# Performance work log

Hardware: AMD Instinct MI355X
Metric: run time of the kernel (lower is better)

## Reference

```python
import jax, jax.numpy as jnp
import numpy as np

# Mamba hyperparams implied by Mamba(d_model=256, d_state=16, d_conv=4), expand=2 default
D_MODEL = 256
D_INNER = 512      # expand * d_model
D_STATE = 16
D_CONV = 4
DT_RANK = 16       # ceil(d_model / 16)
LN_EPS = 1e-5


def setup_inputs() -> dict:
    key = jax.random.key(0)
    ks = jax.random.split(key, 10)
    B, L = 4, 2048
    s = lambda k, shape, sc=0.02: jax.random.normal(k, shape, dtype=jnp.float32) * sc
    x = jax.random.normal(ks[0], (B, L, D_MODEL), dtype=jnp.float32)
    in_proj_w = s(ks[1], (2 * D_INNER, D_MODEL))          # Linear(d_model -> 2*d_inner), no bias
    conv_w = s(ks[2], (D_INNER, 1, D_CONV), 0.1)          # depthwise causal conv
    conv_b = s(ks[3], (D_INNER,), 0.1)
    x_proj_w = s(ks[4], (DT_RANK + 2 * D_STATE, D_INNER))  # Linear(d_inner -> dt_rank+2*d_state), no bias
    dt_proj_w = s(ks[5], (D_INNER, DT_RANK), 0.1)
    dt_proj_b = s(ks[6], (D_INNER,), 0.1)
    # S4D-real init: A_log = log(1..d_state) broadcast over channels
    A_log = jnp.log(jnp.tile(jnp.arange(1, D_STATE + 1, dtype=jnp.float32), (D_INNER, 1)))
    D_param = jnp.ones((D_INNER,), dtype=jnp.float32)
    out_proj_w = s(ks[7], (D_MODEL, D_INNER))             # Linear(d_inner -> d_model), no bias
    ln_w = jnp.ones((D_MODEL,), dtype=jnp.float32)
    ln_b = jnp.zeros((D_MODEL,), dtype=jnp.float32)
    return dict(x=x, in_proj_w=in_proj_w, conv_w=conv_w, conv_b=conv_b,
                x_proj_w=x_proj_w, dt_proj_w=dt_proj_w, dt_proj_b=dt_proj_b,
                A_log=A_log, D_param=D_param, out_proj_w=out_proj_w,
                ln_w=ln_w, ln_b=ln_b)


def _mamba(x, in_proj_w, conv_w, conv_b, x_proj_w, dt_proj_w, dt_proj_b, A_log, D_param, out_proj_w):
    B, L, _ = x.shape
    # input projection -> (x_branch, z_gate), each [B, L, E]
    xz = jnp.einsum('bld,ed->ble', x, in_proj_w)
    xm, z = jnp.split(xz, 2, axis=-1)
    # causal depthwise conv over time: [B, E, L]
    xc = jnp.transpose(xm, (0, 2, 1))
    xc = jax.lax.conv_general_dilated(xc, conv_w, window_strides=(1,),
                                      padding=[(D_CONV - 1, 0)],
                                      feature_group_count=D_INNER)
    xc = jax.nn.silu(xc + conv_b[None, :, None])
    xt = jnp.transpose(xc, (0, 2, 1))                     # [B, L, E]
    # SSM parameter projections
    dbc = jnp.einsum('ble,re->blr', xt, x_proj_w)         # [B, L, R+2N]
    dt, Bm, Cm = jnp.split(dbc, [DT_RANK, DT_RANK + D_STATE], axis=-1)
    delta = jax.nn.softplus(jnp.einsum('blr,er->ble', dt, dt_proj_w) + dt_proj_b)  # [B,L,E]
    A = -jnp.exp(A_log)                                   # [E, N]
    dA = jnp.exp(jnp.einsum('ble,en->blen', delta, A))    # [B,L,E,N]
    dBu = jnp.einsum('ble,bln->blen', delta * xt, Bm)     # [B,L,E,N]

    def step(h, inp):
        dA_t, dBu_t, C_t = inp                            # [B,E,N],[B,E,N],[B,N]
        h = dA_t * h + dBu_t
        y = jnp.einsum('ben,bn->be', h, C_t)
        return h, y

    h0 = jnp.zeros((B, D_INNER, D_STATE), dtype=x.dtype)
    xs = (jnp.moveaxis(dA, 1, 0), jnp.moveaxis(dBu, 1, 0), jnp.moveaxis(Cm, 1, 0))
    _, ys = jax.lax.scan(step, h0, xs)                    # ys: [L, B, E]
    y = jnp.moveaxis(ys, 0, 1) + xt * D_param             # skip term D*u
    y = y * jax.nn.silu(z)                                # gating
    return jnp.einsum('ble,de->bld', y, out_proj_w)


def reference(x, in_proj_w, conv_w, conv_b, x_proj_w, dt_proj_w, dt_proj_b,
              A_log, D_param, out_proj_w, ln_w, ln_b):
    xr = x + _mamba(x, in_proj_w, conv_w, conv_b, x_proj_w, dt_proj_w,
                    dt_proj_b, A_log, D_param, out_proj_w)
    mu = jnp.mean(xr, axis=-1, keepdims=True)
    var = jnp.mean(jnp.square(xr - mu), axis=-1, keepdims=True)
    ln = (xr - mu) * jax.lax.rsqrt(var + LN_EPS) * ln_w + ln_b
    return jnp.transpose(ln, (0, 2, 1))                   # [B, d_model, L]
```

## Files before the change

kernel.cpp:

```cpp
#include <hip/hip_runtime.h>

typedef __attribute__((ext_vector_type(8))) short short8;
typedef __attribute__((ext_vector_type(4))) float f32x4;

#define DMODEL 256
#define DINNER 512
#define NSTATE 16
#define LSEQ   2048
#define NB     4
#define BL     (NB*LSEQ)
#define NCHUNK 128
#define LCHUNK 16

#define NX     (BL*DMODEL)
#define NWIN   (1024*256)
#define NWXP   (64*512)
#define NWOUT  (256*512)

__device__ __forceinline__ ushort f2bf(float f) {
  union { float f; unsigned u; } v; v.f = f;
  unsigned u = v.u;
  unsigned r = (u + 0x7fffu + ((u >> 16) & 1u)) >> 16;
  return (ushort)r;
}
__device__ __forceinline__ float bf2f(ushort u) {
  union { unsigned u; float f; } v; v.u = ((unsigned)u) << 16; return v.f;
}

__device__ __forceinline__ void gld_lds16(const ushort* g, ushort* l) {
  __builtin_amdgcn_global_load_lds(
      (const __attribute__((address_space(1))) void*)g,
      (__attribute__((address_space(3))) void*)l, 16, 0, 0);
}

__global__ __launch_bounds__(256) void cvt_all_k(const float* __restrict__ x,
                                                 const float* __restrict__ w_in,
                                                 const float* __restrict__ w_xp,
                                                 const float* __restrict__ w_out,
                                                 ushort* __restrict__ xbf,
                                                 ushort* __restrict__ winb,
                                                 ushort* __restrict__ wxpb,
                                                 ushort* __restrict__ woutb) {
  int i = blockIdx.x * 256 + threadIdx.x;
  if (i < NX) { xbf[i] = f2bf(x[i]); return; }
  i -= NX;
  if (i < NWIN) { winb[i] = f2bf(w_in[i]); return; }
  i -= NWIN;
  if (i < NWXP) { wxpb[i] = ((i >> 9) < 48) ? f2bf(w_xp[i]) : (ushort)0; return; }
  i -= NWXP;
  if (i < NWOUT) woutb[i] = f2bf(w_out[i]);
}

__device__ __forceinline__ float sp(float s) {
  float ex = __expf(-fabsf(s));
  return fmaxf(s, 0.f) + __logf(1.f + ex);
}

__global__ __launch_bounds__(256) void inproj_conv_k(
    const ushort* __restrict__ A,
    const ushort* __restrict__ W,
    const float* __restrict__ x,
    const float* __restrict__ cw,
    const float* __restrict__ cb,
    ushort* __restrict__ xtbf,
    ushort* __restrict__ zsil) {
  constexpr int BM = 128, BN = 64, K = 256, NT = 4;
  constexpr int AL = BM / 8;
  constexpr int TL = (BM + BN) / 8;
  __shared__ __align__(16) char smem[48 * 1024 + 3 * 64 * 4];
  ushort* lA = (ushort*)smem;
  ushort* lB = (ushort*)(smem + 32768);
  float*  hal = (float*)(smem + 49152);
  const int t    = threadIdx.x;
  const int lane = t & 63;
  const int wave = t >> 6;
  const int wr = (wave >> 1) * 64;
  const int wc = (wave & 1) * 32;
  const int m0 = blockIdx.x * BM;
  const int n0 = blockIdx.y * BN;
  const bool xm_mode = (n0 < DINNER);
  const int lrow = lane >> 3;
  const int lcol = (lane & 7) * 8;

  f32x4 acc[4][2];
#pragma unroll
  for (int i = 0; i < 4; ++i)
#pragma unroll
    for (int j = 0; j < 2; ++j) acc[i][j] = (f32x4){0.f, 0.f, 0.f, 0.f};

  auto stage = [&](int buf, int kt64) {
#pragma unroll
    for (int li = 0; li < TL / 4; ++li) {
      int i = li * 4 + wave;
      if (i < AL) {
        int r = i * 8 + lrow;
        gld_lds16(A + (size_t)(m0 + r) * K + kt64 + lcol, &lA[buf * 8192 + i * 512]);
      } else {
        int r = (i - AL) * 8 + lrow;
        gld_lds16(W + (size_t)(n0 + r) * K + kt64 + lcol, &lB[buf * 4096 + (i - AL) * 512]);
      }
    }
  };

  stage(0, 0);
  if (xm_mode && t < 192) {
    int h = t >> 6, col = t & 63;
    float a = 0.f;
    if ((m0 & (LSEQ - 1)) != 0) {
      const float*  xr = x + (size_t)(m0 - 3 + h) * K;
      const ushort* wrp = W + (size_t)(n0 + col) * K;
      for (int k = 0; k < K; k += 4) {
        float4  xv = *reinterpret_cast<const float4*>(xr + k);
        ushort4 wv = *reinterpret_cast<const ushort4*>(wrp + k);
        a += xv.x * bf2f(wv.x) + xv.y * bf2f(wv.y)
           + xv.z * bf2f(wv.z) + xv.w * bf2f(wv.w);
      }
    }
    hal[h * 64 + col] = a;
  }
  __syncthreads();
  for (int kt = 0; kt < NT; ++kt) {
    const int cur = kt & 1;
    if (kt + 1 < NT) stage(cur ^ 1, (kt + 1) * 64);
#pragma unroll
    for (int kk = 0; kk < 64; kk += 32) {
      const int ko = kk + (lane >> 4) * 8;
      const int rr = lane & 15;
      short8 af[4], bf[2];
#pragma unroll
      for (int i = 0; i < 4; ++i)
        af[i] = *reinterpret_cast<const short8*>(&lA[cur * 8192 + (wr + i * 16 + rr) * 64 + ko]);
#pragma unroll
      for (int j = 0; j < 2; ++j)
        bf[j] = *reinterpret_cast<const short8*>(&lB[cur * 4096 + (wc + j * 16 + rr) * 64 + ko]);
#pragma unroll
      for (int i = 0; i < 4; ++i)
#pragma unroll
        for (int j = 0; j < 2; ++j)
          acc[i][j] = __builtin_amdgcn_mfma_f32_16x16x32_bf16(af[i], bf[j], acc[i][j], 0, 0, 0);
    }
    __syncthreads();
  }
  const int crow = (lane >> 4) * 4;
  const int ccol = lane & 15;

  if (xm_mode) {
    float* tile = (float*)smem;
#pragma unroll
    for (int i = 0; i < 4; ++i)
#pragma unroll
      for (int j = 0; j < 2; ++j)
#pragma unroll
        for (int r = 0; r < 4; ++r)
          tile[(wr + i * 16 + crow + r) * 66 + wc + j * 16 + ccol] = acc[i][j][r];
    __syncthreads();
    const int col = t & 63;
    const int e = n0 + col;
    float4 wq = reinterpret_cast<const float4*>(cw)[e];
    float bias = cb[e];
#pragma unroll 4
    for (int s = 0; s < 32; ++s) {
      int tok = (t >> 6) + s * 4;
      float v0 = tile[tok * 66 + col];
      float v1 = (tok >= 1) ? tile[(tok - 1) * 66 + col] : hal[(tok + 2) * 64 + col];
      float v2 = (tok >= 2) ? tile[(tok - 2) * 66 + col] : hal[(tok + 1) * 64 + col];
      float v3 = (tok >= 3) ? tile[(tok - 3) * 66 + col] : hal[(tok + 0) * 64 + col];
      float sv = bias + v0 * wq.w + v1 * wq.z + v2 * wq.y + v3 * wq.x;
      float sil = sv / (1.f + __expf(-sv));
      xtbf[(size_t)(m0 + tok) * DINNER + e] = f2bf(sil);
    }
  } else {
    const int zc0 = n0 - DINNER;
#pragma unroll
    for (int i = 0; i < 4; ++i)
#pragma unroll
      for (int j = 0; j < 2; ++j) {
        int row = m0 + wr + i * 16 + crow;
        int col = zc0 + wc + j * 16 + ccol;
#pragma unroll
        for (int r = 0; r < 4; ++r) {
          float v = acc[i][j][r];
          zsil[(size_t)(row + r) * DINNER + col] = f2bf(v / (1.f + __expf(-v)));
        }
      }
  }
}

template<int BM, int BN, int WM, int WN, int BF16OUT>
__global__ __launch_bounds__(256) void gemm_db(const ushort* __restrict__ A,
                                               const ushort* __restrict__ W,
                                               void* __restrict__ Cv,
                                               int M, int N, int K) {
  constexpr int FM = BM / WM / 16;
  constexpr int FN = BN / WN / 16;
  constexpr int AL = BM / 8;
  constexpr int TL = (BM + BN) / 8;
  __shared__ __align__(16) ushort lA[2][BM * 64];
  __shared__ __align__(16) ushort lB[2][BN * 64];
  const int t    = threadIdx.x;
  const int lane = t & 63;
  const int wave = t >> 6;
  const int wm = wave / WN, wn = wave % WN;
  const int wr = wm * (BM / WM);
  const int wc = wn * (BN / WN);
  const int m0 = blockIdx.x * BM;
  const int n0 = blockIdx.y * BN;
  const int lrow = lane >> 3;
  const int lcol = (lane & 7) * 8;

  f32x4 acc[FM][FN];
#pragma unroll
  for (int i = 0; i < FM; ++i)
#pragma unroll
    for (int j = 0; j < FN; ++j) acc[i][j] = (f32x4){0.f, 0.f, 0.f, 0.f};

  auto stage = [&](int buf, int kt64) {
#pragma unroll
    for (int li = 0; li < TL / 4; ++li) {
      int i = li * 4 + wave;
      if (i < AL) {
        int r = i * 8 + lrow;
        gld_lds16(A + (size_t)(m0 + r) * K + kt64 + lcol, &lA[buf][i * 512]);
      } else {
        int r = (i - AL) * 8 + lrow;
        gld_lds16(W + (size_t)(n0 + r) * K + kt64 + lcol, &lB[buf][(i - AL) * 512]);
      }
    }
  };

  const int NT = K / 64;
  stage(0, 0);
  __syncthreads();
  for (int kt = 0; kt < NT; ++kt) {
    const int cur = kt & 1;
    if (kt + 1 < NT) stage(cur ^ 1, (kt + 1) * 64);
#pragma unroll
    for (int kk = 0; kk < 64; kk += 32) {
      const int ko = kk + (lane >> 4) * 8;
      const int rr = lane & 15;
      short8 af[FM], bf[FN];
#pragma unroll
      for (int i = 0; i < FM; ++i)
        af[i] = *reinterpret_cast<const short8*>(&lA[cur][(wr + i * 16 + rr) * 64 + ko]);
#pragma unroll
      for (int j = 0; j < FN; ++j)
        bf[j] = *reinterpret_cast<const short8*>(&lB[cur][(wc + j * 16 + rr) * 64 + ko]);
#pragma unroll
      for (int i = 0; i < FM; ++i)
#pragma unroll
        for (int j = 0; j < FN; ++j)
          acc[i][j] = __builtin_amdgcn_mfma_f32_16x16x32_bf16(af[i], bf[j], acc[i][j], 0, 0, 0);
    }
    __syncthreads();
  }
  const int crow = (lane >> 4) * 4;
  const int ccol = lane & 15;
#pragma unroll
  for (int i = 0; i < FM; ++i)
#pragma unroll
    for (int j = 0; j < FN; ++j) {
      int row = m0 + wr + i * 16 + crow;
      int col = n0 + wc + j * 16 + ccol;
      if (BF16OUT) {
        ushort* C = (ushort*)Cv;
#pragma unroll
        for (int r = 0; r < 4; ++r)
          C[(size_t)(row + r) * N + col] = f2bf(acc[i][j][r]);
      } else {
        float* C = (float*)Cv;
#pragma unroll
        for (int r = 0; r < 4; ++r)
          C[(size_t)(row + r) * N + col] = acc[i][j][r];
      }
    }
}

__global__ __launch_bounds__(256) void outproj_ln_tr_k(
    const ushort* __restrict__ A,
    const ushort* __restrict__ W,
    const float* __restrict__ x,
    const float* __restrict__ lw,
    const float* __restrict__ lb,
    float* __restrict__ out) {
  constexpr int BM = 32, BN = 256, K = 512;
  constexpr int FM = 2, FN = 4;
  constexpr int AL = BM / 8;
  constexpr int TL = (BM + BN) / 8;
  __shared__ __align__(16) ushort lA[2][BM * 64];
  __shared__ __align__(16) ushort lB[2][BN * 64];
  const int t    = threadIdx.x;
  const int lane = t & 63;
  const int wave = t >> 6;
  const int wc = wave * 64;
  const int m0 = blockIdx.x * BM;
  const int lrow = lane >> 3;
  const int lcol = (lane & 7) * 8;

  f32x4 acc[FM][FN];
#pragma unroll
  for (int i = 0; i < FM; ++i)
#pragma unroll
    for (int j = 0; j < FN; ++j) acc[i][j] = (f32x4){0.f, 0.f, 0.f, 0.f};

  auto stage = [&](int buf, int kt64) {
#pragma unroll
    for (int li = 0; li < TL / 4; ++li) {
      int i = li * 4 + wave;
      if (i < AL) {
        int r = i * 8 + lrow;
        gld_lds16(A + (size_t)(m0 + r) * K + kt64 + lcol, &lA[buf][i * 512]);
      } else {
        int r = (i - AL) * 8 + lrow;
        gld_lds16(W + (size_t)r * K + kt64 + lcol, &lB[buf][(i - AL) * 512]);
      }
    }
  };

  const int NT = K / 64;
  stage(0, 0);
  __syncthreads();
  for (int kt = 0; kt < NT; ++kt) {
    const int cur = kt & 1;
    if (kt + 1 < NT) stage(cur ^ 1, (kt + 1) * 64);
#pragma unroll
    for (int kk = 0; kk < 64; kk += 32) {
      const int ko = kk + (lane >> 4) * 8;
      const int rr = lane & 15;
      short8 af[FM], bf[FN];
#pragma unroll
      for (int i = 0; i < FM; ++i)
        af[i] = *reinterpret_cast<const short8*>(&lA[cur][(i * 16 + rr) * 64 + ko]);
#pragma unroll
      for (int j = 0; j < FN; ++j)
        bf[j] = *reinterpret_cast<const short8*>(&lB[cur][(wc + j * 16 + rr) * 64 + ko]);
#pragma unroll
      for (int i = 0; i < FM; ++i)
#pragma unroll
        for (int j = 0; j < FN; ++j)
          acc[i][j] = __builtin_amdgcn_mfma_f32_16x16x32_bf16(af[i], bf[j], acc[i][j], 0, 0, 0);
    }
    __syncthreads();
  }

  float (*tile)[257] = reinterpret_cast<float (*)[257]>(&lB[0][0]);
  const int crow = (lane >> 4) * 4;
  const int ccol = lane & 15;
#pragma unroll
  for (int i = 0; i < FM; ++i)
#pragma unroll
    for (int j = 0; j < FN; ++j)
#pragma unroll
      for (int r = 0; r < 4; ++r)
        tile[i * 16 + crow + r][wc + j * 16 + ccol] = acc[i][j][r];
  __syncthreads();

  const int b = m0 / LSEQ, l0 = m0 % LSEQ;
  float4 w4 = *reinterpret_cast<const float4*>(lw + lane * 4);
  float4 b4 = *reinterpret_cast<const float4*>(lb + lane * 4);
#pragma unroll
  for (int s = 0; s < 8; ++s) {
    int row = wave * 8 + s;
    float4 xv = *reinterpret_cast<const float4*>(
        x + ((size_t)(b * LSEQ) + l0 + row) * DMODEL + lane * 4);
    float4 v;
    v.x = xv.x + tile[row][lane * 4 + 0];
    v.y = xv.y + tile[row][lane * 4 + 1];
    v.z = xv.z + tile[row][lane * 4 + 2];
    v.w = xv.w + tile[row][lane * 4 + 3];
    float sm = v.x + v.y + v.z + v.w;
    float ss = v.x * v.x + v.y * v.y + v.z * v.z + v.w * v.w;
#pragma unroll
    for (int o = 1; o < 64; o <<= 1) {
      sm += __shfl_xor(sm, o, 64);
      ss += __shfl_xor(ss, o, 64);
    }
    float mu = sm * (1.f / 256.f);
    float var = ss * (1.f / 256.f) - mu * mu;
    float rs = rsqrtf(var + 1e-5f);
    tile[row][lane * 4 + 0] = (v.x - mu) * rs * w4.x + b4.x;
    tile[row][lane * 4 + 1] = (v.y - mu) * rs * w4.y + b4.y;
    tile[row][lane * 4 + 2] = (v.z - mu) * rs * w4.z + b4.z;
    tile[row][lane * 4 + 3] = (v.w - mu) * rs * w4.w + b4.w;
  }
  __syncthreads();
  int l_i = t & 31;
  int dg = t >> 5;
  size_t ob = (size_t)b * DMODEL * LSEQ + l0 + l_i;
#pragma unroll
  for (int d = dg; d < DMODEL; d += 8)
    out[ob + (size_t)d * LSEQ] = tile[l_i][d];
}

__global__ __launch_bounds__(512) void dlt_k(const float* __restrict__ dbc,
                                             const float* __restrict__ dtw,
                                             const float* __restrict__ dtb,
                                             ushort* __restrict__ dlt) {
  int tg = blockIdx.x;
  int e = threadIdx.x;
  __shared__ float sDt[16][16];
  if (e < 256) {
    int li = e >> 4, n = e & 15;
    sDt[li][n] = dbc[((size_t)tg * 16 + li) * 64 + n];
  }
  const float4* wv = reinterpret_cast<const float4*>(dtw + e * 16);
  float4 w0 = wv[0], w1 = wv[1], w2 = wv[2], w3 = wv[3];
  float bias = dtb[e];
  __syncthreads();
  size_t ob = (size_t)tg * 16 * DINNER + e;
#pragma unroll
  for (int i = 0; i < 16; ++i) {
    float s = bias
      + w0.x*sDt[i][0]  + w0.y*sDt[i][1]  + w0.z*sDt[i][2]  + w0.w*sDt[i][3]
      + w1.x*sDt[i][4]  + w1.y*sDt[i][5]  + w1.z*sDt[i][6]  + w1.w*sDt[i][7]
      + w2.x*sDt[i][8]  + w2.y*sDt[i][9]  + w2.z*sDt[i][10] + w2.w*sDt[i][11]
      + w3.x*sDt[i][12] + w3.y*sDt[i][13] + w3.z*sDt[i][14] + w3.w*sDt[i][15];
    dlt[ob + (size_t)i * DINNER] = f2bf(sp(s));
  }
}

__global__ __launch_bounds__(256) void scanA_k(const ushort* __restrict__ xtbf,
                                               const ushort* __restrict__ dlt,
                                               const float* __restrict__ dbc,
                                               const float* __restrict__ A_log,
                                               ushort* __restrict__ hend,
                                               float* __restrict__ Ssum) {
  int blk = blockIdx.x;
  int half = blk & 1, c = (blk >> 1) & (NCHUNK - 1), b = blk >> 8;
  int e = half * 256 + threadIdx.x;
  __shared__ float sB[LCHUNK][NSTATE];
  {
    int t = threadIdx.x;
    int li = t >> 4, n = t & 15;
    sB[li][n] = dbc[((size_t)(b * LSEQ + c * LCHUNK + li)) * 64 + 16 + n];
  }
  float An0 = -__expf(A_log[e * 16]);
  float h[16];
#pragma unroll
  for (int n = 0; n < 16; ++n) h[n] = 0.f;
  float ssum = 0.f;
  __syncthreads();
  size_t ix = ((size_t)(b * LSEQ + c * LCHUNK)) * DINNER + e;
#pragma unroll
  for (int i = 0; i < LCHUNK; ++i, ix += DINNER) {
    float d = bf2f(dlt[ix]);
    float u = bf2f(xtbf[ix]);
    float du = d * u;
    ssum += d;
    float w = __expf(An0 * d);
    float w2 = w * w, w3 = w2 * w, w4 = w2 * w2;
    float c1 = w, c2 = w2, c3 = w3, c4 = w4;
#pragma unroll
    for (int q = 0; q < 4; ++q) {
      h[q*4+0] = c1 * h[q*4+0] + du * sB[i][q*4+0];
      h[q*4+1] = c2 * h[q*4+1] + du * sB[i][q*4+1];
      h[q*4+2] = c3 * h[q*4+2] + du * sB[i][q*4+2];
      h[q*4+3] = c4 * h[q*4+3] + du * sB[i][q*4+3];
      if (q < 3) { c1 *= w4; c2 *= w4; c3 *= w4; c4 *= w4; }
    }
  }
  size_t ob = ((size_t)b * NCHUNK + c) * DINNER + e;
  ushort tmp[16];
#pragma unroll
  for (int n = 0; n < 16; ++n) tmp[n] = f2bf(h[n]);
  *reinterpret_cast<uint4*>(hend + ob * 16)     = *reinterpret_cast<uint4*>(tmp);
  *reinterpret_cast<uint4*>(hend + ob * 16 + 8) = *reinterpret_cast<uint4*>(tmp + 8);
  Ssum[ob] = ssum;
}

__global__ __launch_bounds__(256) void scanB_k(ushort* hend,
                                               const float* __restrict__ Ssum,
                                               const float* __restrict__ A_log) {
  int idx = blockIdx.x * 256 + threadIdx.x;
  int n = idx & 15, e = (idx >> 4) & (DINNER - 1), b = idx >> 13;
  float An = -__expf(A_log[e * 16 + n]);
  float hc = 0.f;
#pragma unroll 8
  for (int c = 0; c < NCHUNK; ++c) {
    size_t base = ((size_t)b * NCHUNK + c) * DINNER + e;
    float s  = Ssum[base];
    float he = bf2f(hend[base * 16 + n]);
    hend[base * 16 + n] = f2bf(hc);
    hc = __expf(An * s) * hc + he;
  }
}

__global__ __launch_bounds__(256) void scanC_k(const ushort* __restrict__ xtbf,
                                               const ushort* __restrict__ dlt,
                                               const float* __restrict__ dbc,
                                               const float* __restrict__ A_log,
                                               const ushort* __restrict__ hin,
                                               const float* __restrict__ Dp,
                                               const ushort* __restrict__ zsil,
                                               ushort* __restrict__ ybf) {
  int blk = blockIdx.x;
  int half = blk & 1, c = (blk >> 1) & (NCHUNK - 1), b = blk >> 8;
  int e = half * 256 + threadIdx.x;
  __shared__ float sB[LCHUNK][NSTATE];
  __shared__ float sC[LCHUNK][NSTATE];
  {
    int t = threadIdx.x;
    int li = t >> 4, n = t & 15;
    size_t rb = ((size_t)(b * LSEQ + c * LCHUNK + li)) * 64;
    sB[li][n] = dbc[rb + 16 + n];
    sC[li][n] = dbc[rb + 32 + n];
  }
  float An0 = -__expf(A_log[e * 16]);
  float De = Dp[e];
  float h[16];
  size_t ob = ((size_t)b * NCHUNK + c) * DINNER + e;
  {
    uint4 p0 = *reinterpret_cast<const uint4*>(hin + ob * 16);
    uint4 p1 = *reinterpret_cast<const uint4*>(hin + ob * 16 + 8);
    const ushort* tp = reinterpret_cast<const ushort*>(&p0);
#pragma unroll
    for (int n = 0; n < 8; ++n) h[n] = bf2f(tp[n]);
    tp = reinterpret_cast<const ushort*>(&p1);
#pragma unroll
    for (int n = 0; n < 8; ++n) h[8 + n] = bf2f(tp[n]);
  }
  __syncthreads();
  size_t ix = ((size_t)(b * LSEQ + c * LCHUNK)) * DINNER + e;
#pragma unroll
  for (int i = 0; i < LCHUNK; ++i, ix += DINNER) {
    float d = bf2f(dlt[ix]);
    float u = bf2f(xtbf[ix]);
    float du = d * u;
    float w = __expf(An0 * d);
    float w2 = w * w, w3 = w2 * w, w4 = w2 * w2;
    float c1 = w, c2 = w2, c3 = w3, c4 = w4;
    float y0 = 0.f, y1 = 0.f, y2 = 0.f, y3 = 0.f;
#pragma unroll
    for (int q = 0; q < 4; ++q) {
      h[q*4+0] = c1 * h[q*4+0] + du * sB[i][q*4+0];
      h[q*4+1] = c2 * h[q*4+1] + du * sB[i][q*4+1];
      h[q*4+2] = c3 * h[q*4+2] + du * sB[i][q*4+2];
      h[q*4+3] = c4 * h[q*4+3] + du * sB[i][q*4+3];
      y0 += h[q*4+0] * sC[i][q*4+0];
      y1 += h[q*4+1] * sC[i][q*4+1];
      y2 += h[q*4+2] * sC[i][q*4+2];
      y3 += h[q*4+3] * sC[i][q*4+3];
      if (q < 3) { c1 *= w4; c2 *= w4; c3 *= w4; c4 *= w4; }
    }
    float y = ((y0 + y1) + (y2 + y3)) + u * De;
    y *= bf2f(zsil[ix]);
    ybf[ix] = f2bf(y);
  }
}

extern "C" void kernel_launch(void* const* d_in, const int* in_sizes, int n_in,
                              void* d_out, int out_size, void* d_ws, size_t ws_size,
                              hipStream_t stream) {
  const float* x     = (const float*)d_in[0];
  const float* w_in  = (const float*)d_in[1];
  const float* cw    = (const float*)d_in[2];
  const float* cb    = (const float*)d_in[3];
  const float* w_xp  = (const float*)d_in[4];
  const float* dtw   = (const float*)d_in[5];
  const float* dtb   = (const float*)d_in[6];
  const float* A_log = (const float*)d_in[7];
  const float* Dp    = (const float*)d_in[8];
  const float* w_out = (const float*)d_in[9];
  const float* lw    = (const float*)d_in[10];
  const float* lb    = (const float*)d_in[11];
  float* out = (float*)d_out;

  char* ws = (char*)d_ws;
  size_t off = 0;
  auto alloc = [&](size_t bytes) -> char* {
    char* p = ws + off;
    off += (bytes + 255) & ~(size_t)255;
    return p;
  };
  ushort* xbf   = (ushort*)alloc((size_t)BL * DMODEL * 2);
  ushort* winb  = (ushort*)alloc((size_t)1024 * 256 * 2);
  ushort* wxpb  = (ushort*)alloc((size_t)64 * 512 * 2);
  ushort* woutb = (ushort*)alloc((size_t)256 * 512 * 2);
  ushort* xtbf  = (ushort*)alloc((size_t)BL * DINNER * 2);
  ushort* zsil  = (ushort*)alloc((size_t)BL * DINNER * 2);
  float*  dbc   = (float*) alloc((size_t)BL * 64 * 4);
  ushort* dlt   = (ushort*)alloc((size_t)BL * DINNER * 2);
  float*  Ssum  = (float*) alloc((size_t)NB * NCHUNK * DINNER * 4);
  ushort* hend  = (ushort*)alloc((size_t)NB * NCHUNK * DINNER * NSTATE * 2);
  ushort* ybf   = (ushort*)alloc((size_t)BL * DINNER * 2);

  cvt_all_k<<<dim3((NX + NWIN + NWXP + NWOUT + 255) / 256), dim3(256), 0, stream>>>(
      x, w_in, w_xp, w_out, xbf, winb, wxpb, woutb);

  inproj_conv_k<<<dim3(BL / 128, 1024 / 64), dim3(256), 0, stream>>>(
      xbf, winb, x, cw, cb, xtbf, zsil);

  gemm_db<32, 64, 1, 4, 0><<<dim3(BL / 32, 1), dim3(256), 0, stream>>>(
      xtbf, wxpb, dbc, BL, 64, 512);

  dlt_k<<<dim3(BL / 16), dim3(512), 0, stream>>>(dbc, dtw, dtb, dlt);

  scanA_k<<<dim3(NB * NCHUNK * 2), dim3(256), 0, stream>>>(xtbf, dlt, dbc, A_log, hend, Ssum);
  scanB_k<<<dim3(NB * DINNER * NSTATE / 256), dim3(256), 0, stream>>>(hend, Ssum, A_log);
  scanC_k<<<dim3(NB * NCHUNK * 2), dim3(256), 0, stream>>>(xtbf, dlt, dbc, A_log, hend, Dp, zsil, ybf);

  outproj_ln_tr_k<<<dim3(BL / 32), dim3(256), 0, stream>>>(
      ybf, woutb, x, lw, lb, out);
}
```

Measured before the change: 99.19 us.

## Fuse x_proj GEMM with dt projection and pack delta with u for scans

Replaces the separate x_proj GEMM and dt-projection kernels with one kernel. It computes the dt/B/C projection, keeps the dt-rank slice in shared memory, and applies the dt_proj linear plus softplus in the same block. The delta value is packed with the bf16 input u into a single 32-bit word, so both scan kernels issue one load per element instead of two. This saves a kernel launch and the round trip of dbc through global memory for dt. In exchange, each block does more serial work (64 tokens per thread), and the fused kernel now reads xtbf again to build the packed buffer.

```diff
diff --git a/kernel.cpp b/kernel.cpp
--- a/kernel.cpp
+++ b/kernel.cpp
@@ -186,33 +186,31 @@
   }
 }
 
-template<int BM, int BN, int WM, int WN, int BF16OUT>
-__global__ __launch_bounds__(256) void gemm_db(const ushort* __restrict__ A,
-                                               const ushort* __restrict__ W,
-                                               void* __restrict__ Cv,
-                                               int M, int N, int K) {
-  constexpr int FM = BM / WM / 16;
-  constexpr int FN = BN / WN / 16;
+__global__ __launch_bounds__(256) void xproj_dlt_k(
+    const ushort* __restrict__ A,
+    const ushort* __restrict__ W,
+    float* __restrict__ dbc,
+    const float* __restrict__ dtw,
+    const float* __restrict__ dtb,
+    const ushort* __restrict__ xtbf,
+    unsigned* __restrict__ dux) {
+  constexpr int BM = 32, BN = 64, K = 512, NT = 8;
   constexpr int AL = BM / 8;
   constexpr int TL = (BM + BN) / 8;
   __shared__ __align__(16) ushort lA[2][BM * 64];
   __shared__ __align__(16) ushort lB[2][BN * 64];
+  __shared__ float sDt[BM][16];
   const int t    = threadIdx.x;
   const int lane = t & 63;
   const int wave = t >> 6;
-  const int wm = wave / WN, wn = wave % WN;
-  const int wr = wm * (BM / WM);
-  const int wc = wn * (BN / WN);
+  const int wc = wave * 16;
   const int m0 = blockIdx.x * BM;
-  const int n0 = blockIdx.y * BN;
   const int lrow = lane >> 3;
   const int lcol = (lane & 7) * 8;
 
-  f32x4 acc[FM][FN];
-#pragma unroll
-  for (int i = 0; i < FM; ++i)
-#pragma unroll
-    for (int j = 0; j < FN; ++j) acc[i][j] = (f32x4){0.f, 0.f, 0.f, 0.f};
+  f32x4 acc[2][1];
+#pragma unroll
+  for (int i = 0; i < 2; ++i) acc[i][0] = (f32x4){0.f, 0.f, 0.f, 0.f};
 
   auto stage = [&](int buf, int kt64) {
 #pragma unroll
@@ -223,12 +221,11 @@
         gld_lds16(A + (size_t)(m0 + r) * K + kt64 + lcol, &lA[buf][i * 512]);
       } else {
         int r = (i - AL) * 8 + lrow;
-        gld_lds16(W + (size_t)(n0 + r) * K + kt64 + lcol, &lB[buf][(i - AL) * 512]);
+        gld_lds16(W + (size_t)r * K + kt64 + lcol, &lB[buf][(i - AL) * 512]);
       }
     }
   };
 
-  const int NT = K / 64;
   stage(0, 0);
   __syncthreads();
   for (int kt = 0; kt < NT; ++kt) {
@@ -238,41 +235,53 @@
     for (int kk = 0; kk < 64; kk += 32) {
       const int ko = kk + (lane >> 4) * 8;
       const int rr = lane & 15;
-      short8 af[FM], bf[FN];
-#pragma unroll
-      for (int i = 0; i < FM; ++i)
-        af[i] = *reinterpret_cast<const short8*>(&lA[cur][(wr + i * 16 + rr) * 64 + ko]);
-#pragma unroll
-      for (int j = 0; j < FN; ++j)
-        bf[j] = *reinterpret_cast<const short8*>(&lB[cur][(wc + j * 16 + rr) * 64 + ko]);
-#pragma unroll
-      for (int i = 0; i < FM; ++i)
-#pragma unroll
-        for (int j = 0; j < FN; ++j)
-          acc[i][j] = __builtin_amdgcn_mfma_f32_16x16x32_bf16(af[i], bf[j], acc[i][j], 0, 0, 0);
+      short8 af[2], bf;
+#pragma unroll
+      for (int i = 0; i < 2; ++i)
+        af[i] = *reinterpret_cast<const short8*>(&lA[cur][(i * 16 + rr) * 64 + ko]);
+      bf = *reinterpret_cast<const short8*>(&lB[cur][(wc + rr) * 64 + ko]);
+#pragma unroll
+      for (int i = 0; i < 2; ++i)
+        acc[i][0] = __builtin_amdgcn_mfma_f32_16x16x32_bf16(af[i], bf, acc[i][0], 0, 0, 0);
     }
     __syncthreads();
   }
   const int crow = (lane >> 4) * 4;
   const int ccol = lane & 15;
 #pragma unroll
-  for (int i = 0; i < FM; ++i)
-#pragma unroll
-    for (int j = 0; j < FN; ++j) {
-      int row = m0 + wr + i * 16 + crow;
-      int col = n0 + wc + j * 16 + ccol;
-      if (BF16OUT) {
-        ushort* C = (ushort*)Cv;
-#pragma unroll
-        for (int r = 0; r < 4; ++r)
-          C[(size_t)(row + r) * N + col] = f2bf(acc[i][j][r]);
-      } else {
-        float* C = (float*)Cv;
-#pragma unroll
-        for (int r = 0; r < 4; ++r)
-          C[(size_t)(row + r) * N + col] = acc[i][j][r];
-      }
-    }
+  for (int i = 0; i < 2; ++i) {
+    int row = m0 + i * 16 + crow;
+    int col = wc + ccol;
+#pragma unroll
+    for (int r = 0; r < 4; ++r)
+      dbc[(size_t)(row + r) * 64 + col] = acc[i][0][r];
+  }
+  if (wave == 0) {
+#pragma unroll
+    for (int i = 0; i < 2; ++i)
+#pragma unroll
+      for (int r = 0; r < 4; ++r)
+        sDt[i * 16 + crow + r][ccol] = acc[i][0][r];
+  }
+  __syncthreads();
+#pragma unroll
+  for (int s = 0; s < 2; ++s) {
+    int e = s * 256 + t;
+    const float4* wv = reinterpret_cast<const float4*>(dtw + e * 16);
+    float4 w0 = wv[0], w1 = wv[1], w2 = wv[2], w3 = wv[3];
+    float bias = dtb[e];
+#pragma unroll 4
+    for (int tok = 0; tok < BM; ++tok) {
+      float sv = bias
+        + w0.x*sDt[tok][0]  + w0.y*sDt[tok][1]  + w0.z*sDt[tok][2]  + w0.w*sDt[tok][3]
+        + w1.x*sDt[tok][4]  + w1.y*sDt[tok][5]  + w1.z*sDt[tok][6]  + w1.w*sDt[tok][7]
+        + w2.x*sDt[tok][8]  + w2.y*sDt[tok][9]  + w2.z*sDt[tok][10] + w2.w*sDt[tok][11]
+        + w3.x*sDt[tok][12] + w3.y*sDt[tok][13] + w3.z*sDt[tok][14] + w3.w*sDt[tok][15];
+      size_t ix = (size_t)(m0 + tok) * DINNER + e;
+      unsigned pack = (unsigned)f2bf(sp(sv)) | ((unsigned)xtbf[ix] << 16);
+      dux[ix] = pack;
+    }
+  }
 }
 
 __global__ __launch_bounds__(256) void outproj_ln_tr_k(
@@ -391,35 +400,7 @@
     out[ob + (size_t)d * LSEQ] = tile[l_i][d];
 }
 
-__global__ __launch_bounds__(512) void dlt_k(const float* __restrict__ dbc,
-                                             const float* __restrict__ dtw,
-                                             const float* __restrict__ dtb,
-                                             ushort* __restrict__ dlt) {
-  int tg = blockIdx.x;
-  int e = threadIdx.x;
-  __shared__ float sDt[16][16];
-  if (e < 256) {
-    int li = e >> 4, n = e & 15;
-    sDt[li][n] = dbc[((size_t)tg * 16 + li) * 64 + n];
-  }
-  const float4* wv = reinterpret_cast<const float4*>(dtw + e * 16);
-  float4 w0 = wv[0], w1 = wv[1], w2 = wv[2], w3 = wv[3];
-  float bias = dtb[e];
-  __syncthreads();
-  size_t ob = (size_t)tg * 16 * DINNER + e;
-#pragma unroll
-  for (int i = 0; i < 16; ++i) {
-    float s = bias
-      + w0.x*sDt[i][0]  + w0.y*sDt[i][1]  + w0.z*sDt[i][2]  + w0.w*sDt[i][3]
-      + w1.x*sDt[i][4]  + w1.y*sDt[i][5]  + w1.z*sDt[i][6]  + w1.w*sDt[i][7]
-      + w2.x*sDt[i][8]  + w2.y*sDt[i][9]  + w2.z*sDt[i][10] + w2.w*sDt[i][11]
-      + w3.x*sDt[i][12] + w3.y*sDt[i][13] + w3.z*sDt[i][14] + w3.w*sDt[i][15];
-    dlt[ob + (size_t)i * DINNER] = f2bf(sp(s));
-  }
-}
-
-__global__ __launch_bounds__(256) void scanA_k(const ushort* __restrict__ xtbf,
-                                               const ushort* __restrict__ dlt,
+__global__ __launch_bounds__(256) void scanA_k(const unsigned* __restrict__ dux,
                                                const float* __restrict__ dbc,
                                                const float* __restrict__ A_log,
                                                ushort* __restrict__ hend,
@@ -442,8 +423,9 @@
   size_t ix = ((size_t)(b * LSEQ + c * LCHUNK)) * DINNER + e;
 #pragma unroll
   for (int i = 0; i < LCHUNK; ++i, ix += DINNER) {
-    float d = bf2f(dlt[ix]);
-    float u = bf2f(xtbf[ix]);
+    unsigned pk = dux[ix];
+    float d = bf2f((ushort)(pk & 0xffffu));
+    float u = bf2f((ushort)(pk >> 16));
     float du = d * u;
     ssum += d;
     float w = __expf(An0 * d);
@@ -484,8 +466,7 @@
   }
 }
 
-__global__ __launch_bounds__(256) void scanC_k(const ushort* __restrict__ xtbf,
-                                               const ushort* __restrict__ dlt,
+__global__ __launch_bounds__(256) void scanC_k(const unsigned* __restrict__ dux,
                                                const float* __restrict__ dbc,
                                                const float* __restrict__ A_log,
                                                const ushort* __restrict__ hin,
@@ -522,8 +503,9 @@
   size_t ix = ((size_t)(b * LSEQ + c * LCHUNK)) * DINNER + e;
 #pragma unroll
   for (int i = 0; i < LCHUNK; ++i, ix += DINNER) {
-    float d = bf2f(dlt[ix]);
-    float u = bf2f(xtbf[ix]);
+    unsigned pk = dux[ix];
+    float d = bf2f((ushort)(pk & 0xffffu));
+    float u = bf2f((ushort)(pk >> 16));
     float du = d * u;
     float w = __expf(An0 * d);
     float w2 = w * w, w3 = w2 * w, w4 = w2 * w2;
@@ -571,17 +553,17 @@
     off += (bytes + 255) & ~(size_t)255;
     return p;
   };
-  ushort* xbf   = (ushort*)alloc((size_t)BL * DMODEL * 2);
-  ushort* winb  = (ushort*)alloc((size_t)1024 * 256 * 2);
-  ushort* wxpb  = (ushort*)alloc((size_t)64 * 512 * 2);
-  ushort* woutb = (ushort*)alloc((size_t)256 * 512 * 2);
-  ushort* xtbf  = (ushort*)alloc((size_t)BL * DINNER * 2);
-  ushort* zsil  = (ushort*)alloc((size_t)BL * DINNER * 2);
-  float*  dbc   = (float*) alloc((size_t)BL * 64 * 4);
-  ushort* dlt   = (ushort*)alloc((size_t)BL * DINNER * 2);
-  float*  Ssum  = (float*) alloc((size_t)NB * NCHUNK * DINNER * 4);
-  ushort* hend  = (ushort*)alloc((size_t)NB * NCHUNK * DINNER * NSTATE * 2);
-  ushort* ybf   = (ushort*)alloc((size_t)BL * DINNER * 2);
+  ushort*   xbf   = (ushort*)alloc((size_t)BL * DMODEL * 2);
+  ushort*   winb  = (ushort*)alloc((size_t)1024 * 256 * 2);
+  ushort*   wxpb  = (ushort*)alloc((size_t)64 * 512 * 2);
+  ushort*   woutb = (ushort*)alloc((size_t)256 * 512 * 2);
+  ushort*   xtbf  = (ushort*)alloc((size_t)BL * DINNER * 2);
+  ushort*   zsil  = (ushort*)alloc((size_t)BL * DINNER * 2);
+  float*    dbc   = (float*) alloc((size_t)BL * 64 * 4);
+  unsigned* dux   = (unsigned*)alloc((size_t)BL * DINNER * 4);
+  float*    Ssum  = (float*) alloc((size_t)NB * NCHUNK * DINNER * 4);
+  ushort*   hend  = (ushort*)alloc((size_t)NB * NCHUNK * DINNER * NSTATE * 2);
+  ushort*   ybf   = (ushort*)alloc((size_t)BL * DINNER * 2);
 
   cvt_all_k<<<dim3((NX + NWIN + NWXP + NWOUT + 255) / 256), dim3(256), 0, stream>>>(
       x, w_in, w_xp, w_out, xbf, winb, wxpb, woutb);
@@ -589,14 +571,12 @@
   inproj_conv_k<<<dim3(BL / 128, 1024 / 64), dim3(256), 0, stream>>>(
       xbf, winb, x, cw, cb, xtbf, zsil);
 
-  gemm_db<32, 64, 1, 4, 0><<<dim3(BL / 32, 1), dim3(256), 0, stream>>>(
-      xtbf, wxpb, dbc, BL, 64, 512);
-
-  dlt_k<<<dim3(BL / 16), dim3(512), 0, stream>>>(dbc, dtw, dtb, dlt);
-
-  scanA_k<<<dim3(NB * NCHUNK * 2), dim3(256), 0, stream>>>(xtbf, dlt, dbc, A_log, hend, Ssum);
+  xproj_dlt_k<<<dim3(BL / 32), dim3(256), 0, stream>>>(
+      xtbf, wxpb, dbc, dtw, dtb, xtbf, dux);
+
+  scanA_k<<<dim3(NB * NCHUNK * 2), dim3(256), 0, stream>>>(dux, dbc, A_log, hend, Ssum);
   scanB_k<<<dim3(NB * DINNER * NSTATE / 256), dim3(256), 0, stream>>>(hend, Ssum, A_log);
-  scanC_k<<<dim3(NB * NCHUNK * 2), dim3(256), 0, stream>>>(xtbf, dlt, dbc, A_log, hend, Dp, zsil, ybf);
+  scanC_k<<<dim3(NB * NCHUNK * 2), dim3(256), 0, stream>>>(dux, dbc, A_log, hend, Dp, zsil, ybf);
 
   outproj_ln_tr_k<<<dim3(BL / 32), dim3(256), 0, stream>>>(
       ybf, woutb, x, lw, lb, out);
```

Measured after the change: 93.75 us. -5.5%, faster.
